# Kernel optimization log

Hardware: AMD Instinct MI355X
Metric: run time of the kernel (lower is better)

## Reference

```python
import jax, jax.numpy as jnp
import numpy as np

B, T, E, H = 2, 2048, 1024, 4
Dk = E // H          # 256 head qk dim
Dv = Dk * 2          # 512 head v dim (expansion_ratio=2)
EPS = 1e-5
ROPE_BASE = 10000.0


def setup_inputs() -> dict:
    key = jax.random.key(0)
    ks = jax.random.split(key, 7)
    s = 0.02  # small init matching xavier gains in reset_parameters
    return {
        "x": jax.random.normal(ks[0], (B, T, E), jnp.float32),
        "Wq": jax.random.normal(ks[1], (E, E), jnp.float32) * s,
        "Wk": jax.random.normal(ks[2], (E, E), jnp.float32) * s,
        "Wv": jax.random.normal(ks[3], (E, 2 * E), jnp.float32) * s,
        "Wg": jax.random.normal(ks[4], (E, 2 * E), jnp.float32) * s,
        "Wo": jax.random.normal(ks[5], (2 * E, E), jnp.float32) * s,
        "gn_weight": jnp.ones((Dv,), jnp.float32),
    }


def _rotary(q, k):
    # q,k: [b, t, h, d]; non-interleaved (GPT-NeoX) rotary over the full head dim
    d = q.shape[-1]
    inv_freq = 1.0 / (ROPE_BASE ** (jnp.arange(0, d, 2, dtype=jnp.float32) / d))
    t = jnp.arange(q.shape[1], dtype=jnp.float32)
    freqs = jnp.einsum('t,f->tf', t, inv_freq)      # [t, d/2]
    cos = jnp.cos(freqs)[None, :, None, :]
    sin = jnp.sin(freqs)[None, :, None, :]

    def rot(x):
        x1, x2 = x[..., : d // 2], x[..., d // 2:]
        return jnp.concatenate([x1 * cos - x2 * sin, x2 * cos + x1 * sin], axis=-1)

    return rot(q), rot(k)


def reference(x, Wq, Wk, Wv, Wg, Wo, gn_weight):
    b, t, e = x.shape
    q = (x @ Wq).reshape(b, t, H, Dk)
    k = (x @ Wk).reshape(b, t, H, Dk)
    q, k = _rotary(q, k)
    q = q.transpose(0, 2, 1, 3) * (Dk ** -0.5)      # [b,h,t,dk], scale = head_qk_dim^-0.5
    k = k.transpose(0, 2, 1, 3)
    v = (x @ Wv).reshape(b, t, H, Dv).transpose(0, 2, 1, 3)  # [b,h,t,dv]

    # RetNet per-head decay: gamma_h = 1 - 2^-(5+h)
    gamma = 1.0 - jnp.exp2(-5.0 - jnp.arange(H, dtype=jnp.float32))
    ti = jnp.arange(t)
    n = ti[:, None] - ti[None, :]                   # t - s
    decay = jnp.where(
        n >= 0,
        gamma[:, None, None] ** jnp.maximum(n, 0).astype(jnp.float32),
        0.0,
    )                                               # [h,t,t] causal decayed mask

    scores = jnp.einsum('bhtd,bhsd->bhts', q, k) * decay[None]
    o = jnp.einsum('bhts,bhsd->bhtd', scores, v)    # [b,h,t,dv]
    o = o.transpose(0, 2, 1, 3)                     # [b,t,h,dv]

    # per-head RMSNorm (group_norm over head_v_dim)
    rms = jnp.sqrt(jnp.mean(o * o, axis=-1, keepdims=True) + EPS)
    o = o / rms * gn_weight

    # NOTE: the given source multiplies by raw g_proj(x) (gate_fn not applied in forward)
    g = x @ Wg                                      # [b,t,2E]
    return (o.reshape(b, t, H * Dv) * g) @ Wo       # [b,t,E]
```

## Files before the change

### kernel.cpp

```cpp
#include <hip/hip_runtime.h>
#include <hip/hip_bf16.h>

#define B_ 2
#define T_ 2048
#define E_ 1024
#define DK 256
#define DV 512
#define MROWS 4096
#define LDQKVG 6144
#define CHK 128
#define NCHK 16

typedef __attribute__((ext_vector_type(8))) short short8;
typedef __attribute__((ext_vector_type(4))) short short4v;
typedef __attribute__((ext_vector_type(4))) float floatx4;

typedef __attribute__((address_space(3))) unsigned as3_u32;
typedef const __attribute__((address_space(1))) unsigned as1_u32;

static __device__ __forceinline__ void gld_lds16(const unsigned short* gsrc, unsigned short* ldst) {
  __builtin_amdgcn_global_load_lds((as1_u32*)gsrc, (as3_u32*)ldst, 16, 0, 0);
}

static __device__ __forceinline__ float bf2f(unsigned short u) {
  union { unsigned int i; float f; } x; x.i = ((unsigned int)u) << 16; return x.f;
}
static __device__ __forceinline__ unsigned short f2bf(float f) {
  __hip_bfloat16 h = __float2bfloat16(f);
  return __builtin_bit_cast(unsigned short, h);
}
static __device__ __forceinline__ float load_as_f(const float* p) { return *p; }
static __device__ __forceinline__ float load_as_f(const unsigned short* p) { return bf2f(*p); }

__global__ void __launch_bounds__(256) convx_kernel(const float* __restrict__ x,
                                                    unsigned short* __restrict__ xb) {
  int i = blockIdx.x * 256 + threadIdx.x;
  size_t base = (size_t)i * 8;
  float4 a = *(const float4*)(x + base);
  float4 b = *(const float4*)(x + base + 4);
  short8 o;
  o[0] = (short)f2bf(a.x); o[1] = (short)f2bf(a.y);
  o[2] = (short)f2bf(a.z); o[3] = (short)f2bf(a.w);
  o[4] = (short)f2bf(b.x); o[5] = (short)f2bf(b.y);
  o[6] = (short)f2bf(b.z); o[7] = (short)f2bf(b.w);
  *(short8*)(xb + base) = o;
}

template<typename TIN>
__global__ void __launch_bounds__(256) transpose_bf16_kernel(
    const TIN* __restrict__ in, int ldin, unsigned short* __restrict__ out, int ldout) {
  __shared__ float tile[32][33];
  int c0 = blockIdx.x * 32, r0 = blockIdx.y * 32;
  int tx = threadIdx.x & 31, ty = threadIdx.x >> 5;
#pragma unroll
  for (int i = 0; i < 32; i += 8)
    tile[ty + i][tx] = load_as_f(&in[(size_t)(r0 + ty + i) * ldin + c0 + tx]);
  __syncthreads();
#pragma unroll
  for (int i = 0; i < 32; i += 8)
    out[(size_t)(c0 + ty + i) * ldout + r0 + tx] = f2bf(tile[tx][ty + i]);
}

__global__ void __launch_bounds__(256) kts_transpose_kernel(
    const unsigned short* __restrict__ in, unsigned short* __restrict__ out) {
  __shared__ float tile[32][33];
  int c0 = blockIdx.x * 32, r0 = blockIdx.y * 32;
  int tx = threadIdx.x & 31, ty = threadIdx.x >> 5;
#pragma unroll
  for (int i = 0; i < 32; i += 8)
    tile[ty + i][tx] = bf2f(in[(size_t)(r0 + ty + i) * LDQKVG + c0 + tx]);
  __syncthreads();
  int h = c0 >> 8;
  float lg = log2f(1.0f - exp2f(-5.0f - (float)h));
  int t = r0 + tx;
  float fac = exp2f((float)(CHK - (t & (CHK - 1))) * lg);
#pragma unroll
  for (int i = 0; i < 32; i += 8)
    out[(size_t)(c0 + ty + i) * MROWS + r0 + tx] = f2bf(tile[tx][ty + i] * fac);
}

template<int MTILE, bool F32OUT>
static __device__ __forceinline__ void gemm_tile(
    const unsigned short* __restrict__ A, int lda,
    const unsigned short* __restrict__ Bt, int ldb,
    int K, char* __restrict__ Cbase, int ldc) {
  __shared__ unsigned short As[MTILE * 32];
  __shared__ unsigned short Bs[128 * 32];
  constexpr int MB = MTILE / 32;
  constexpr int AJ = MTILE / 64;
  const int tid = threadIdx.x;
  const int lane = tid & 63;
  const int wid = tid >> 6;
  const int wr = (wid >> 1) * (MTILE / 2), wc = (wid & 1) * 64;
  floatx4 acc[MB][4];
#pragma unroll
  for (int i = 0; i < MB; i++)
#pragma unroll
    for (int j = 0; j < 4; j++)
      acc[i][j] = (floatx4){0.f, 0.f, 0.f, 0.f};

  for (int k0 = 0; k0 < K; k0 += 32) {
    __syncthreads();
#pragma unroll
    for (int j = 0; j < AJ; ++j) {
      int ci = (wid * AJ + j) * 64 + lane;
      int row = ci >> 2, cc = (ci & 3) * 8;
      gld_lds16(&A[(size_t)row * lda + k0 + cc], &As[(wid * AJ + j) * 512]);
    }
#pragma unroll
    for (int j = 0; j < 2; ++j) {
      int ci = (wid * 2 + j) * 64 + lane;
      int row = ci >> 2, cc = (ci & 3) * 8;
      gld_lds16(&Bt[(size_t)row * ldb + k0 + cc], &Bs[(wid * 2 + j) * 512]);
    }
    __syncthreads();
    short8 af[MB], bfr[4];
#pragma unroll
    for (int mb = 0; mb < MB; mb++)
      af[mb] = *(const short8*)&As[(wr + mb * 16 + (lane & 15)) * 32 + (lane >> 4) * 8];
#pragma unroll
    for (int nb = 0; nb < 4; nb++)
      bfr[nb] = *(const short8*)&Bs[(wc + nb * 16 + (lane & 15)) * 32 + (lane >> 4) * 8];
#pragma unroll
    for (int mb = 0; mb < MB; mb++)
#pragma unroll
      for (int nb = 0; nb < 4; nb++)
        acc[mb][nb] = __builtin_amdgcn_mfma_f32_16x16x32_bf16(af[mb], bfr[nb], acc[mb][nb], 0, 0, 0);
  }
#pragma unroll
  for (int mb = 0; mb < MB; mb++)
#pragma unroll
    for (int nb = 0; nb < 4; nb++)
#pragma unroll
      for (int r = 0; r < 4; r++) {
        int row = wr + mb * 16 + (lane >> 4) * 4 + r;
        int col = wc + nb * 16 + (lane & 15);
        float v = acc[mb][nb][r];
        if (F32OUT) ((float*)Cbase)[(size_t)row * ldc + col] = v;
        else ((unsigned short*)Cbase)[(size_t)row * ldc + col] = f2bf(v);
      }
}

template<int MTILE, bool F32OUT>
__global__ void __launch_bounds__(256) gemm_bt_kernel(
    const unsigned short* __restrict__ A, int lda,
    const unsigned short* __restrict__ Bt, int ldb, int K,
    void* __restrict__ Cp, int ldc, int ccol0) {
  size_t m0 = (size_t)blockIdx.x * MTILE;
  size_t n0 = (size_t)blockIdx.y * 128;
  size_t esz = F32OUT ? 4 : 2;
  gemm_tile<MTILE, F32OUT>(A + m0 * lda, lda, Bt + n0 * ldb, ldb, K,
                           (char*)Cp + esz * (m0 * ldc + ccol0 + n0), ldc);
}

__global__ void __launch_bounds__(256) rope_kernel(unsigned short* __restrict__ qkvg) {
  int idx = blockIdx.x * 256 + threadIdx.x;
  int j = idx & 127;
  int h = (idx >> 7) & 3;
  int row = idx >> 9;
  int t = row & (T_ - 1);
  float invf = exp2f(-(float)j * (13.287712379549449f / 128.0f));
  float ang = (float)t * invf;
  float c = cosf(ang), s = sinf(ang);
  float lg = log2f(1.0f - exp2f(-5.0f - (float)h));
  float sq = 0.0625f * exp2f((float)(t & (CHK - 1)) * lg);
  size_t base = (size_t)row * LDQKVG + h * DK + j;
  float q1 = bf2f(qkvg[base]), q2 = bf2f(qkvg[base + 128]);
  float k1 = bf2f(qkvg[base + E_]), k2 = bf2f(qkvg[base + E_ + 128]);
  qkvg[base]            = f2bf((q1 * c - q2 * s) * sq);
  qkvg[base + 128]      = f2bf((q2 * c + q1 * s) * sq);
  qkvg[base + E_]       = f2bf(k1 * c - k2 * s);
  qkvg[base + E_ + 128] = f2bf(k2 * c + k1 * s);
}

__global__ void __launch_bounds__(256) state_kernel(
    const unsigned short* __restrict__ kTs, const unsigned short* __restrict__ vT,
    unsigned short* __restrict__ Sbuf) {
  const int lane = threadIdx.x & 63, wid = threadIdx.x >> 6;
  const int bh = blockIdx.x & 7, dkt = (blockIdx.x >> 3) & 3, dvt = (blockIdx.x >> 5) & 15;
  const int b = bh >> 2, h = bh & 3;
  const float lg = log2f(1.0f - exp2f(-5.0f - (float)h));
  const float g128 = exp2f((float)CHK * lg);
  const int dk0 = dkt * 64 + wid * 16;
  const int dv0 = dvt * 32;
  const unsigned short* arow = kTs + (size_t)(h * DK + dk0 + (lane & 15)) * MROWS + b * T_ + (lane >> 4) * 8;
  const unsigned short* brow = vT + (size_t)(h * DV + dv0 + (lane & 15)) * MROWS + b * T_ + (lane >> 4) * 8;
  floatx4 acc[2];
  acc[0] = (floatx4){0.f, 0.f, 0.f, 0.f};
  acc[1] = (floatx4){0.f, 0.f, 0.f, 0.f};
#pragma unroll 1
  for (int c = 0; c < NCHK; ++c) {
    size_t sb = (size_t)(c * 8 + bh) * (DV * DK);
#pragma unroll
    for (int nb = 0; nb < 2; ++nb) {
      short4v o;
#pragma unroll
      for (int r = 0; r < 4; ++r) o[r] = (short)f2bf(acc[nb][r]);
      *(short4v*)&Sbuf[sb + (size_t)(dv0 + nb * 16 + (lane & 15)) * DK + dk0 + (lane >> 4) * 4] = o;
    }
#pragma unroll
    for (int nb = 0; nb < 2; ++nb)
#pragma unroll
      for (int r = 0; r < 4; ++r) acc[nb][r] *= g128;
#pragma unroll
    for (int ks = 0; ks < 4; ++ks) {
      short8 a = *(const short8*)(arow + c * CHK + ks * 32);
#pragma unroll
      for (int nb = 0; nb < 2; ++nb) {
        short8 bb = *(const short8*)(brow + (size_t)nb * 16 * MROWS + c * CHK + ks * 32);
        acc[nb] = __builtin_amdgcn_mfma_f32_16x16x32_bf16(a, bb, acc[nb], 0, 0, 0);
      }
    }
  }
}

__global__ void __launch_bounds__(256) retention2_kernel(
    const unsigned short* __restrict__ qkvg, const unsigned short* __restrict__ vT,
    const unsigned short* __restrict__ Sbuf, const float* __restrict__ gnw,
    unsigned short* __restrict__ og, float* __restrict__ ssbuf) {
  __shared__ unsigned short k_lds[2][32 * 256];
  __shared__ unsigned short v_lds[2][256 * 32];
  __shared__ unsigned short s_lds[4][16 * 40];
  const int tid = threadIdx.x, lane = tid & 63, wid = tid >> 6;
  const int bh  = blockIdx.x & 7;
  const int c   = (blockIdx.x >> 3) & 15;
  const int dvh = (blockIdx.x >> 7) & 1;
  const int rhf = (blockIdx.x >> 8) & 1;
  const int b = bh >> 2, h = bh & 3;
  const float lg = log2f(1.0f - exp2f(-5.0f - (float)h));
  const int rb0 = b * T_ + c * CHK + rhf * 64;
  const int taub = rhf * 64 + wid * 16;
  const int nst = rhf ? 4 : 2;
  const unsigned short* kbase = qkvg + (size_t)(b * T_ + c * CHK) * LDQKVG + E_ + h * DK;
  const unsigned short* vbase = vT + (size_t)(h * DV + dvh * 256) * MROWS + b * T_ + c * CHK;
  const unsigned short* Sp = Sbuf + (size_t)(c * 8 + bh) * (DV * DK) + (size_t)dvh * 256 * DK;

  auto stage = [&](int buf, int st) {
    int s0 = st * 32;
#pragma unroll
    for (int j = 0; j < 4; ++j) {
      int ci = (wid * 4 + j) * 64 + lane;
      int row = ci >> 5, cc = ci & 31;
      int cs = cc ^ (row & 7);
      gld_lds16(kbase + (size_t)(s0 + row) * LDQKVG + cs * 8, &k_lds[buf][(wid * 4 + j) * 512]);
    }
#pragma unroll
    for (int j = 0; j < 4; ++j) {
      int ci = (wid * 4 + j) * 64 + lane;
      int dv = ci >> 2, cc = ci & 3;
      int cs = cc ^ ((dv ^ (dv >> 2)) & 3);
      gld_lds16(vbase + (size_t)dv * MROWS + s0 + cs * 8, &v_lds[buf][(wid * 4 + j) * 512]);
    }
  };

  stage(0, 0);

  short8 qf[8];
  {
    int qrow = rb0 + wid * 16 + (lane & 15);
    const unsigned short* qp = qkvg + (size_t)qrow * LDQKVG + h * DK + (lane >> 4) * 8;
#pragma unroll
    for (int kk = 0; kk < 8; kk++) qf[kk] = *(const short8*)(qp + kk * 32);
  }
  floatx4 oacc[16];
#pragma unroll
  for (int nb = 0; nb < 16; ++nb) oacc[nb] = (floatx4){0.f, 0.f, 0.f, 0.f};
#pragma unroll
  for (int ks = 0; ks < 8; ++ks) {
#pragma unroll
    for (int nb = 0; nb < 16; ++nb) {
      short8 sf = *(const short8*)&Sp[(size_t)(nb * 16 + (lane & 15)) * DK + ks * 32 + (lane >> 4) * 8];
      oacc[nb] = __builtin_amdgcn_mfma_f32_16x16x32_bf16(qf[ks], sf, oacc[nb], 0, 0, 0);
    }
  }

#pragma unroll 1
  for (int st = 0; st < nst; ++st) {
    const int cur = st & 1;
    __syncthreads();
    if (st + 1 < nst) stage(cur ^ 1, st + 1);
#pragma unroll
    for (int ch = 0; ch < 2; ++ch) {
      floatx4 f = (floatx4){0.f, 0.f, 0.f, 0.f};
      const int srow = ch * 16 + (lane & 15);
#pragma unroll
      for (int kk = 0; kk < 8; kk++) {
        int cc = (kk * 4 + (lane >> 4)) ^ (srow & 7);
        short8 kf = *(const short8*)&k_lds[cur][srow * 256 + cc * 8];
        f = __builtin_amdgcn_mfma_f32_16x16x32_bf16(qf[kk], kf, f, 0, 0, 0);
      }
#pragma unroll
      for (int r = 0; r < 4; ++r) {
        int lr = (lane >> 4) * 4 + r;
        int sig = st * 32 + ch * 16 + (lane & 15);
        int n = taub + lr - sig;
        float val = (n >= 0) ? f[r] * exp2f(-(float)sig * lg) : 0.0f;
        s_lds[wid][lr * 40 + ch * 16 + (lane & 15)] = f2bf(val);
      }
    }
    short8 af = *(const short8*)&s_lds[wid][(lane & 15) * 40 + (lane >> 4) * 8];
#pragma unroll
    for (int nb = 0; nb < 16; ++nb) {
      int dv = nb * 16 + (lane & 15);
      int cc = (lane >> 4) ^ ((dv ^ (dv >> 2)) & 3);
      short8 vf = *(const short8*)&v_lds[cur][dv * 32 + cc * 8];
      oacc[nb] = __builtin_amdgcn_mfma_f32_16x16x32_bf16(af, vf, oacc[nb], 0, 0, 0);
    }
  }
#pragma unroll
  for (int r = 0; r < 4; ++r) {
    float ss = 0.f;
#pragma unroll
    for (int nb = 0; nb < 16; nb++) { float xv = oacc[nb][r]; ss += xv * xv; }
    ss += __shfl_xor(ss, 1, 64);
    ss += __shfl_xor(ss, 2, 64);
    ss += __shfl_xor(ss, 4, 64);
    ss += __shfl_xor(ss, 8, 64);
    if ((lane & 15) == 0) {
      int row = rb0 + wid * 16 + (lane >> 4) * 4 + r;
      ssbuf[(size_t)row * 8 + h * 2 + dvh] = ss;
    }
  }
#pragma unroll
  for (int r = 0; r < 4; ++r) {
    int row = rb0 + wid * 16 + (lane >> 4) * 4 + r;
    size_t growbase = (size_t)row * LDQKVG + 4096 + h * DV + dvh * 256;
    size_t orowbase = (size_t)row * LDQKVG + h * DV + dvh * 256;
#pragma unroll
    for (int nb = 0; nb < 16; nb++) {
      int col = nb * 16 + (lane & 15);
      float gv = bf2f(qkvg[growbase + col]);
      og[orowbase + col] = f2bf(oacc[nb][r] * gnw[dvh * 256 + col] * gv);
    }
  }
}

__global__ void __launch_bounds__(256) normalize_kernel(
    unsigned short* __restrict__ og, const float* __restrict__ ssbuf) {
  int i = blockIdx.x * 256 + threadIdx.x;
  size_t e0 = (size_t)i * 8;
  int row = (int)(e0 >> 11);
  int col = (int)(e0 & 2047);
  int h = col >> 9;
  float ss = ssbuf[(size_t)row * 8 + h * 2] + ssbuf[(size_t)row * 8 + h * 2 + 1];
  float inv = rsqrtf(ss * (1.0f / 512.0f) + 1e-5f);
  size_t a = (size_t)row * LDQKVG + col;
  short8 v = *(const short8*)(og + a);
#pragma unroll
  for (int j = 0; j < 8; j++) v[j] = (short)f2bf(bf2f((unsigned short)v[j]) * inv);
  *(short8*)(og + a) = v;
}

extern "C" void kernel_launch(void* const* d_in, const int* in_sizes, int n_in,
                              void* d_out, int out_size, void* d_ws, size_t ws_size,
                              hipStream_t stream) {
  const float* x   = (const float*)d_in[0];
  const float* Wq  = (const float*)d_in[1];
  const float* Wk  = (const float*)d_in[2];
  const float* Wv  = (const float*)d_in[3];
  const float* Wg  = (const float*)d_in[4];
  const float* Wo  = (const float*)d_in[5];
  const float* gnw = (const float*)d_in[6];
  float* out = (float*)d_out;

  char* ws = (char*)d_ws;
  size_t off = 0;
  auto alloc = [&](size_t bytes) { char* p = ws + off; off += (bytes + 255) & ~(size_t)255; return p; };
  unsigned short* qkvg = (unsigned short*)alloc((size_t)MROWS * LDQKVG * 2);
  unsigned short* vT   = (unsigned short*)alloc((size_t)2048 * MROWS * 2);
  char* regS = alloc((size_t)NCHK * 8 * DV * DK * 2);
  unsigned short* Sbuf  = (unsigned short*)regS;
  unsigned short* xb    = (unsigned short*)regS;
  unsigned short* WallT = (unsigned short*)(regS + 8388608);
  char* regK = alloc((size_t)1024 * MROWS * 2);
  unsigned short* kTs = (unsigned short*)regK;
  unsigned short* WoT = (unsigned short*)regK;
  float* ssbuf = (float*)alloc((size_t)MROWS * 8 * 4);
  unsigned short* og = qkvg + 2048;

  convx_kernel<<<2048, 256, 0, stream>>>(x, xb);

  transpose_bf16_kernel<float><<<dim3(32, 32), 256, 0, stream>>>(Wq, 1024, WallT, 1024);
  transpose_bf16_kernel<float><<<dim3(32, 32), 256, 0, stream>>>(Wk, 1024, WallT + (size_t)1024 * 1024, 1024);
  transpose_bf16_kernel<float><<<dim3(64, 32), 256, 0, stream>>>(Wv, 2048, WallT + (size_t)2048 * 1024, 1024);
  transpose_bf16_kernel<float><<<dim3(64, 32), 256, 0, stream>>>(Wg, 2048, WallT + (size_t)4096 * 1024, 1024);

  gemm_bt_kernel<128, false><<<dim3(32, 48), 256, 0, stream>>>(xb, 1024, WallT, 1024, 1024, qkvg, LDQKVG, 0);

  rope_kernel<<<8192, 256, 0, stream>>>(qkvg);

  kts_transpose_kernel<<<dim3(32, 128), 256, 0, stream>>>(qkvg + E_, kTs);

  transpose_bf16_kernel<unsigned short><<<dim3(64, 128), 256, 0, stream>>>(qkvg + 2048, LDQKVG, vT, MROWS);

  state_kernel<<<512, 256, 0, stream>>>(kTs, vT, Sbuf);

  transpose_bf16_kernel<float><<<dim3(32, 64), 256, 0, stream>>>(Wo, 1024, WoT, 2048);

  retention2_kernel<<<512, 256, 0, stream>>>(qkvg, vT, Sbuf, gnw, og, ssbuf);

  normalize_kernel<<<4096, 256, 0, stream>>>(og, ssbuf);

  gemm_bt_kernel<64, true><<<dim3(64, 8), 256, 0, stream>>>(og, LDQKVG, WoT, 2048, 2048, out, E_, 0);
}
```

Baseline: 253.0 us.

## Add triple-buffered 128x256 GEMM for QKVG projection and merge weight transposes

```diff
diff --git a/kernel.cpp b/kernel.cpp
--- a/kernel.cpp
+++ b/kernel.cpp
@@ -61,6 +61,28 @@
     out[(size_t)(c0 + ty + i) * ldout + r0 + tx] = f2bf(tile[tx][ty + i]);
 }
 
+__global__ void __launch_bounds__(256) transpose_weights_kernel(
+    const float* __restrict__ Wq, const float* __restrict__ Wk,
+    const float* __restrict__ Wv, const float* __restrict__ Wg,
+    unsigned short* __restrict__ out) {
+  __shared__ float tile[32][33];
+  int bid = blockIdx.x;
+  const float* in; unsigned short* o; int ldin, nbx;
+  if (bid < 1024)      { in = Wq; o = out;                       ldin = 1024; nbx = 32; }
+  else if (bid < 2048) { in = Wk; o = out + (size_t)1024 * 1024; ldin = 1024; nbx = 32; bid -= 1024; }
+  else if (bid < 4096) { in = Wv; o = out + (size_t)2048 * 1024; ldin = 2048; nbx = 64; bid -= 2048; }
+  else                 { in = Wg; o = out + (size_t)4096 * 1024; ldin = 2048; nbx = 64; bid -= 4096; }
+  int c0 = (bid % nbx) * 32, r0 = (bid / nbx) * 32;
+  int tx = threadIdx.x & 31, ty = threadIdx.x >> 5;
+#pragma unroll
+  for (int i = 0; i < 32; i += 8)
+    tile[ty + i][tx] = in[(size_t)(r0 + ty + i) * ldin + c0 + tx];
+  __syncthreads();
+#pragma unroll
+  for (int i = 0; i < 32; i += 8)
+    o[(size_t)(c0 + ty + i) * 1024 + r0 + tx] = f2bf(tile[tx][ty + i]);
+}
+
 __global__ void __launch_bounds__(256) kts_transpose_kernel(
     const unsigned short* __restrict__ in, unsigned short* __restrict__ out) {
   __shared__ float tile[32][33];
@@ -77,6 +99,101 @@
 #pragma unroll
   for (int i = 0; i < 32; i += 8)
     out[(size_t)(c0 + ty + i) * MROWS + r0 + tx] = f2bf(tile[tx][ty + i] * fac);
+}
+
+template<int BM, int BN, int KK, bool F32OUT>
+__global__ void __launch_bounds__(512, 4) gemm3_kernel(
+    const unsigned short* __restrict__ A, int lda,
+    const unsigned short* __restrict__ Bt, int ldb,
+    void* __restrict__ Cp, int ldc, int ccol0) {
+  constexpr int NT = KK / 32;
+  constexpr int AG = BM / 128;
+  constexpr int BG = BN / 128;
+  __shared__ __align__(16) unsigned short lds[3][(BM + BN) * 32];
+  const int tid = threadIdx.x;
+  const int lane = tid & 63;
+  const int wid = tid >> 6;
+  const int wm = wid >> 2, wn = wid & 3;
+  const int m0 = blockIdx.x * BM;
+  const int n0 = blockIdx.y * BN;
+  const unsigned short* Ab = A + (size_t)m0 * lda;
+  const unsigned short* Bb = Bt + (size_t)n0 * ldb;
+
+  auto stage = [&](int sl, int t) {
+    const int k0 = t * 32;
+#pragma unroll
+    for (int j = 0; j < AG; ++j) {
+      int g = wid * AG + j;
+      int ci = g * 64 + lane;
+      int row = ci >> 2, c = ci & 3;
+      int cs = c ^ ((row >> 1) & 3);
+      gld_lds16(Ab + (size_t)row * lda + k0 + cs * 8, &lds[sl][g * 512]);
+    }
+#pragma unroll
+    for (int j = 0; j < BG; ++j) {
+      int g = wid * BG + j;
+      int ci = g * 64 + lane;
+      int row = ci >> 2, c = ci & 3;
+      int cs = c ^ ((row >> 1) & 3);
+      gld_lds16(Bb + (size_t)row * ldb + k0 + cs * 8, &lds[sl][BM * 32 + g * 512]);
+    }
+  };
+
+  floatx4 acc[4][4];
+#pragma unroll
+  for (int i = 0; i < 4; i++)
+#pragma unroll
+    for (int j = 0; j < 4; j++)
+      acc[i][j] = (floatx4){0.f, 0.f, 0.f, 0.f};
+
+  stage(0, 0);
+  stage(1, 1);
+
+  int cur = 0;
+#pragma unroll 1
+  for (int t = 0; t < NT; ++t) {
+    if (t + 1 < NT) {
+      if constexpr (AG + BG == 3) asm volatile("s_waitcnt vmcnt(3)" ::: "memory");
+      else if constexpr (AG + BG == 2) asm volatile("s_waitcnt vmcnt(2)" ::: "memory");
+      else asm volatile("s_waitcnt vmcnt(4)" ::: "memory");
+    } else {
+      asm volatile("s_waitcnt vmcnt(0)" ::: "memory");
+    }
+    __builtin_amdgcn_s_barrier();
+    asm volatile("" ::: "memory");
+    int sl = cur + 2; if (sl >= 3) sl -= 3;
+    if (t + 2 < NT) stage(sl, t + 2);
+
+    const unsigned short* As_ = lds[cur];
+    const unsigned short* Bs_ = lds[cur] + BM * 32;
+    short8 af[4], bfv[4];
+#pragma unroll
+    for (int i = 0; i < 4; ++i) {
+      int row = wm * 64 + i * 16 + (lane & 15);
+      af[i] = *(const short8*)&As_[row * 32 + (((lane >> 4) ^ ((row >> 1) & 3)) * 8)];
+      int nn = wn * 64 + i * 16 + (lane & 15);
+      bfv[i] = *(const short8*)&Bs_[nn * 32 + (((lane >> 4) ^ ((nn >> 1) & 3)) * 8)];
+    }
+#pragma unroll
+    for (int i = 0; i < 4; ++i)
+#pragma unroll
+      for (int j = 0; j < 4; ++j)
+        acc[i][j] = __builtin_amdgcn_mfma_f32_16x16x32_bf16(af[i], bfv[j], acc[i][j], 0, 0, 0);
+    cur = cur + 1 == 3 ? 0 : cur + 1;
+  }
+
+#pragma unroll
+  for (int i = 0; i < 4; ++i)
+#pragma unroll
+    for (int j = 0; j < 4; ++j)
+#pragma unroll
+      for (int r = 0; r < 4; ++r) {
+        int row = m0 + wm * 64 + i * 16 + (lane >> 4) * 4 + r;
+        int col = ccol0 + n0 + wn * 64 + j * 16 + (lane & 15);
+        float v = acc[i][j][r];
+        if (F32OUT) ((float*)Cp)[(size_t)row * ldc + col] = v;
+        else ((unsigned short*)Cp)[(size_t)row * ldc + col] = f2bf(v);
+      }
 }
 
 template<int MTILE, bool F32OUT>
@@ -380,12 +497,10 @@
 
   convx_kernel<<<2048, 256, 0, stream>>>(x, xb);
 
-  transpose_bf16_kernel<float><<<dim3(32, 32), 256, 0, stream>>>(Wq, 1024, WallT, 1024);
-  transpose_bf16_kernel<float><<<dim3(32, 32), 256, 0, stream>>>(Wk, 1024, WallT + (size_t)1024 * 1024, 1024);
-  transpose_bf16_kernel<float><<<dim3(64, 32), 256, 0, stream>>>(Wv, 2048, WallT + (size_t)2048 * 1024, 1024);
-  transpose_bf16_kernel<float><<<dim3(64, 32), 256, 0, stream>>>(Wg, 2048, WallT + (size_t)4096 * 1024, 1024);
-
-  gemm_bt_kernel<128, false><<<dim3(32, 48), 256, 0, stream>>>(xb, 1024, WallT, 1024, 1024, qkvg, LDQKVG, 0);
+  transpose_weights_kernel<<<6144, 256, 0, stream>>>(Wq, Wk, Wv, Wg, WallT);
+
+  gemm3_kernel<128, 256, 1024, false><<<dim3(32, 24), 512, 0, stream>>>(
+      xb, 1024, WallT, 1024, qkvg, LDQKVG, 0);
 
   rope_kernel<<<8192, 256, 0, stream>>>(qkvg);
 
```

Result: faster. 237.3 us (-6.2%).
